# Optimization experiments

Measured on AMD Instinct MI355X. Metric: run time of the kernel, lower is better.

The kernel has to match this reference:

```python
import jax, jax.numpy as jnp
import numpy as np

PATCH = (9, 7, 5, 3)
DIM = 64
HEAD_DIM = 64
HEADS = 8
HIDDEN = 8
DEPTH = 4
SCALE = (HEAD_DIM / HEADS) ** (-0.5)  # per-head dim = 8
EPS = 1e-5


def setup_inputs() -> dict:
    key = jax.random.key(0)
    ks = jax.random.split(key, 8)
    B = 4096
    x = jax.random.normal(ks[0], (B, PATCH[0] * PATCH[0], DIM), dtype=jnp.float32)
    w_qkv = jax.random.normal(ks[1], (DEPTH, DIM, 3 * HEAD_DIM), dtype=jnp.float32) * 0.05
    b_qkv = jnp.zeros((DEPTH, 3 * HEAD_DIM), dtype=jnp.float32)
    w_o = jax.random.normal(ks[2], (DEPTH, HEAD_DIM, DIM), dtype=jnp.float32) * 0.05
    b_o = jnp.zeros((DEPTH, DIM), dtype=jnp.float32)
    ln1_g = jnp.ones((DEPTH, DIM), dtype=jnp.float32)
    ln1_b = jnp.zeros((DEPTH, DIM), dtype=jnp.float32)
    ln2_g = jnp.ones((DEPTH, DIM), dtype=jnp.float32)
    ln2_b = jnp.zeros((DEPTH, DIM), dtype=jnp.float32)
    w1 = jax.random.normal(ks[3], (DEPTH, DIM, HIDDEN), dtype=jnp.float32) * 0.05
    b1 = jnp.zeros((DEPTH, HIDDEN), dtype=jnp.float32)
    w2 = jax.random.normal(ks[4], (DEPTH, HIDDEN, DIM), dtype=jnp.float32) * 0.05
    b2 = jnp.zeros((DEPTH, DIM), dtype=jnp.float32)
    return {"x": x, "w_qkv": w_qkv, "b_qkv": b_qkv, "w_o": w_o, "b_o": b_o,
            "ln1_g": ln1_g, "ln1_b": ln1_b, "ln2_g": ln2_g, "ln2_b": ln2_b,
            "w1": w1, "b1": b1, "w2": w2, "b2": b2}


def _layernorm(x, g, b):
    m = jnp.mean(x, axis=-1, keepdims=True)
    v = jnp.mean(jnp.square(x - m), axis=-1, keepdims=True)
    return (x - m) * jax.lax.rsqrt(v + EPS) * g + b


def reference(x, w_qkv, b_qkv, w_o, b_o, ln1_g, ln1_b, ln2_g, ln2_b, w1, b1, w2, b2):
    B = x.shape[0]
    for i in range(DEPTH):
        n = x.shape[1]
        # --- attention block (Residual(Layernorm(Encoder))) ---
        y = _layernorm(x, ln1_g[i], ln1_b[i])
        qkv = y @ w_qkv[i] + b_qkv[i]                       # [B, n, 3*HEAD_DIM]
        q, k, v = jnp.split(qkv, 3, axis=-1)
        dh = HEAD_DIM // HEADS                              # 8
        q = q.reshape(B, n, HEADS, dh)
        k = k.reshape(B, n, HEADS, dh)
        v = v.reshape(B, n, HEADS, dh)
        dots = jnp.einsum('bihd,bjhd->bhij', q, k) * SCALE  # [B, H, n, n]
        attn = jax.nn.softmax(dots, axis=-1)
        out = jnp.einsum('bhij,bjhd->bihd', attn, v).reshape(B, n, HEAD_DIM)
        out = out @ w_o[i] + b_o[i]
        x = x + out                                         # dropout = identity (eval)
        # --- feedforward block ---
        y = _layernorm(x, ln2_g[i], ln2_b[i])
        h = jax.nn.gelu(y @ w1[i] + b1[i], approximate=False)
        x = x + h @ w2[i] + b2[i]
        # --- spatial pooling / rearrange ---
        p = PATCH[i]
        xg = x.reshape(B, p, p, DIM)                        # 'b (h w) d -> b h w d'
        if i != DEPTH - 1:
            xg = xg[:, 1:-1, 1:-1, :]                       # crop pool_size=1
            x = xg.reshape(B, (p - 2) * (p - 2), DIM)
        else:
            x = jnp.transpose(xg, (0, 3, 1, 2))             # 'b h w d -> b d h w'
    return x  # [B, 64, 3, 3]
```

## Files before the change

kernel.cpp:

```cpp
#include <hip/hip_runtime.h>
#include <hip/hip_bf16.h>
#include <math.h>

#define NT 512

typedef __attribute__((ext_vector_type(8))) short short8v;
typedef __attribute__((ext_vector_type(4))) short short4v;
typedef __attribute__((ext_vector_type(4))) float f32x4;
typedef __attribute__((ext_vector_type(2))) unsigned uint2v;
typedef __attribute__((ext_vector_type(4))) unsigned uint4v;

__device__ __forceinline__ unsigned short f2bf(float x) {
    unsigned u = __float_as_uint(x);
    unsigned r = ((u >> 16) & 1u) + 0x7FFFu;
    return (unsigned short)((u + r) >> 16);
}
__device__ __forceinline__ unsigned pk2(float a, float b) {
    __hip_bfloat162 h = __float22bfloat162_rn(make_float2(a, b));
    unsigned r;
    __builtin_memcpy(&r, &h, sizeof(r));
    return r;
}
__device__ __forceinline__ short bf1(float a) {
    __hip_bfloat16 h = __float2bfloat16(a);
    short r;
    __builtin_memcpy(&r, &h, sizeof(r));
    return r;
}
__device__ __forceinline__ float gelu_f(float x) {
    float x3 = x * x * x;
    float e = exp2f(-2.3022079f * x - 0.1029432f * x3);
    return x / (1.0f + e);
}
__device__ __forceinline__ f32x4 mfma32(short8v a, short8v b, f32x4 c) {
    return __builtin_amdgcn_mfma_f32_16x16x32_bf16(a, b, c, 0, 0, 0);
}

#define WS_WO 49152
#define WS_W1 65536
#define WS_W2 69632
#define WS_TOT 71680

__global__ __launch_bounds__(256) void prep_kernel(
    const float* __restrict__ w_qkv, const float* __restrict__ w_o,
    const float* __restrict__ w1, const float* __restrict__ w2,
    short* __restrict__ ws)
{
    int idx = blockIdx.x * 256 + threadIdx.x;
    if (idx < WS_WO) {
        int l = idx / 12288, r = idx % 12288, c = r >> 6, d = r & 63;
        ws[idx] = (short)f2bf(w_qkv[l * 12288 + d * 192 + c]);
    } else if (idx < WS_W1) {
        int k = idx - WS_WO; int l = k / 4096, r = k % 4096, c = r >> 6, d = r & 63;
        ws[idx] = (short)f2bf(w_o[l * 4096 + d * 64 + c]);
    } else if (idx < WS_W2) {
        int k = idx - WS_W1; int l = k / 1024, r = k % 1024, j = r >> 6, d = r & 63;
        ws[idx] = (j < 8) ? (short)f2bf(w1[l * 512 + d * 8 + j]) : (short)0;
    } else if (idx < WS_TOT) {
        int k = idx - WS_W2; int l = k / 512, r = k % 512, c = r >> 3, j = r & 7;
        ws[idx] = (short)f2bf(w2[l * 512 + j * 64 + c]);
    }
}

template<int N, int P, int L, bool LAST>
__device__ __forceinline__ void layer_fn(
    float* __restrict__ xs, short* __restrict__ ybf, short* __restrict__ qbf,
    short* __restrict__ kbf, short* __restrict__ vT,
    const short* __restrict__ ws,
    const float* __restrict__ b_qkv, const float* __restrict__ b_o,
    const float* __restrict__ ln1_g, const float* __restrict__ ln1_b,
    const float* __restrict__ ln2_g, const float* __restrict__ ln2_b,
    const float* __restrict__ b1,    const float* __restrict__ b2,
    float* __restrict__ out, int b, int t)
{
    constexpr int Mt = (N + 15) / 16;
    constexpr float SC = 0.35355339059327373f;
    const int wv = t >> 6, l = t & 63, lr = l & 15, lq = l >> 4;
    short8v zero8 = {};
    f32x4 zero4 = {0.f, 0.f, 0.f, 0.f};

    if (t < 64 * Mt) {
        const int token = t >> 2, part = t & 3, d0 = part * 16;
        short* yrow = ybf + token * 72 + d0;
        if (token < N) {
            const int row = (token / P + L) * 9 + token % P + L;
            const float* xr = xs + row * 68 + d0;
            f32x4 v[4];
            #pragma unroll
            for (int k = 0; k < 4; ++k) v[k] = *(const f32x4*)(xr + 4 * k);
            float s1 = 0.f, s2 = 0.f;
            #pragma unroll
            for (int k = 0; k < 4; ++k)
                #pragma unroll
                for (int e = 0; e < 4; ++e) { s1 += v[k][e]; s2 += v[k][e] * v[k][e]; }
            s1 += __shfl_xor(s1, 1); s2 += __shfl_xor(s2, 1);
            s1 += __shfl_xor(s1, 2); s2 += __shfl_xor(s2, 2);
            const float m = s1 * 0.015625f;
            const float r = rsqrtf(s2 * 0.015625f - m * m + 1e-5f);
            uint4v w0, w1v;
            #pragma unroll
            for (int k = 0; k < 4; ++k) {
                f32x4 g  = *(const f32x4*)&ln1_g[L * 64 + d0 + 4 * k];
                f32x4 bb = *(const f32x4*)&ln1_b[L * 64 + d0 + 4 * k];
                unsigned p0 = pk2((v[k][0]-m)*r*g[0]+bb[0], (v[k][1]-m)*r*g[1]+bb[1]);
                unsigned p1 = pk2((v[k][2]-m)*r*g[2]+bb[2], (v[k][3]-m)*r*g[3]+bb[3]);
                if (k == 0) { w0.x = p0; w0.y = p1; }
                else if (k == 1) { w0.z = p0; w0.w = p1; }
                else if (k == 2) { w1v.x = p0; w1v.y = p1; }
                else { w1v.z = p0; w1v.w = p1; }
            }
            *(uint4v*)yrow = w0;
            *(uint4v*)(yrow + 8) = w1v;
        } else {
            uint4v z = {};
            *(uint4v*)yrow = z;
            *(uint4v*)(yrow + 8) = z;
        }
    }
    __syncthreads();

    {
        const short* wqL = ws + L * 12288;
        for (int u = wv; u < Mt * 12; u += 8) {
            const int mt = u / 12, ct = u - mt * 12;
            const short* yr = &ybf[(16 * mt + lr) * 72 + lq * 8];
            short8v y0 = *(const short8v*)yr, y1 = *(const short8v*)(yr + 32);
            const short* wr = &wqL[(16 * ct + lr) * 64 + lq * 8];
            short8v w0 = *(const short8v*)wr, w1 = *(const short8v*)(wr + 32);
            if (ct < 8) {
                f32x4 acc = mfma32(w0, y0, zero4);
                acc = mfma32(w1, y1, acc);
                f32x4 bq = *(const f32x4*)&b_qkv[L * 192 + 16 * ct + lq * 4];
                const int i = 16 * mt + lr;
                if (ct < 4) {
                    unsigned p0 = pk2((acc[0]+bq[0])*SC, (acc[1]+bq[1])*SC);
                    unsigned p1 = pk2((acc[2]+bq[2])*SC, (acc[3]+bq[3])*SC);
                    unsigned* dst = (unsigned*)&qbf[i * 72 + 16 * ct + lq * 4];
                    dst[0] = p0; dst[1] = p1;
                } else {
                    unsigned p0 = pk2(acc[0]+bq[0], acc[1]+bq[1]);
                    unsigned p1 = pk2(acc[2]+bq[2], acc[3]+bq[3]);
                    unsigned* dst = (unsigned*)&kbf[i * 72 + 16 * (ct - 4) + lq * 4];
                    dst[0] = p0; dst[1] = p1;
                }
            } else {
                f32x4 acc = mfma32(y0, w0, zero4);
                acc = mfma32(y1, w1, acc);
                const int cv = 16 * (ct - 8) + lr;
                const float bias = b_qkv[L * 192 + 128 + cv];
                unsigned p0 = pk2(acc[0]+bias, acc[1]+bias);
                unsigned p1 = pk2(acc[2]+bias, acc[3]+bias);
                unsigned* dst = (unsigned*)&vT[cv * 104 + 16 * mt + lq * 4];
                dst[0] = p0; dst[1] = p1;
            }
        }
    }
    __syncthreads();

    {
        const int h = wv, hh = wv >> 1;
        short8v kf[Mt];
        #pragma unroll
        for (int jt = 0; jt < Mt; ++jt)
            kf[jt] = (l < 16) ? *(const short8v*)&kbf[(16 * jt + lr) * 72 + h * 8] : zero8;
#if __has_builtin(__builtin_amdgcn_mfma_f32_16x16x16bf16_1k)
        short4v vf[Mt];
        #pragma unroll
        for (int jt = 0; jt < Mt; ++jt)
            vf[jt] = *(const short4v*)&vT[(16 * hh + lr) * 104 + 16 * jt + lq * 4];
#else
        constexpr int KS2 = (Mt + 1) / 2;
        short8v vf8[KS2];
        #pragma unroll
        for (int ks = 0; ks < KS2; ++ks)
            vf8[ks] = *(const short8v*)&vT[(16 * hh + lr) * 104 + 32 * ks + lq * 8];
#endif
        for (int mt = 0; mt < Mt; ++mt) {
            short8v bq = (l < 16) ? *(const short8v*)&qbf[(16 * mt + lr) * 72 + h * 8] : zero8;
            f32x4 acc[Mt];
            #pragma unroll
            for (int jt = 0; jt < Mt; ++jt) acc[jt] = mfma32(kf[jt], bq, zero4);
            float psum = 0.f;
            #pragma unroll
            for (int jt = 0; jt < Mt; ++jt) {
                #pragma unroll
                for (int rg = 0; rg < 4; ++rg) {
                    const int j = 16 * jt + lq * 4 + rg;
                    float e = __expf(acc[jt][rg]);
                    e = (j < N) ? e : 0.f;
                    acc[jt][rg] = e;
                    psum += e;
                }
            }
            float den = psum + __shfl_xor(psum, 16);
            den += __shfl_xor(den, 32);
            const float dinv = 1.0f / den;
            unsigned pkk[Mt][2];
            #pragma unroll
            for (int jt = 0; jt < Mt; ++jt) {
                pkk[jt][0] = pk2(acc[jt][0] * dinv, acc[jt][1] * dinv);
                pkk[jt][1] = pk2(acc[jt][2] * dinv, acc[jt][3] * dinv);
            }
            f32x4 po = zero4;
#if __has_builtin(__builtin_amdgcn_mfma_f32_16x16x16bf16_1k)
            #pragma unroll
            for (int jt = 0; jt < Mt; ++jt) {
                uint2v pw; pw.x = pkk[jt][0]; pw.y = pkk[jt][1];
                short4v bv = __builtin_bit_cast(short4v, pw);
                po = __builtin_amdgcn_mfma_f32_16x16x16bf16_1k(vf[jt], bv, po, 0, 0, 0);
            }
#else
            #pragma unroll
            for (int ks = 0; ks < KS2; ++ks) {
                const int t1ok = (2 * ks + 1) < Mt;
                unsigned pA0 = pkk[2 * ks][0], pA1 = pkk[2 * ks][1];
                unsigned pB0 = t1ok ? pkk[2 * ks + 1][0] : 0u;
                unsigned pB1 = t1ok ? pkk[2 * ks + 1][1] : 0u;
                int i01 = ((((lq & 1) * 2) * 16) + lr) * 4;
                int i23 = ((((lq & 1) * 2 + 1) * 16) + lr) * 4;
                unsigned w0a = (unsigned)__builtin_amdgcn_ds_bpermute(i01, (int)pA0);
                unsigned w0b = (unsigned)__builtin_amdgcn_ds_bpermute(i01, (int)pB0);
                unsigned w1a = (unsigned)__builtin_amdgcn_ds_bpermute(i01, (int)pA1);
                unsigned w1b = (unsigned)__builtin_amdgcn_ds_bpermute(i01, (int)pB1);
                unsigned w2a = (unsigned)__builtin_amdgcn_ds_bpermute(i23, (int)pA0);
                unsigned w2b = (unsigned)__builtin_amdgcn_ds_bpermute(i23, (int)pB0);
                unsigned w3a = (unsigned)__builtin_amdgcn_ds_bpermute(i23, (int)pA1);
                unsigned w3b = (unsigned)__builtin_amdgcn_ds_bpermute(i23, (int)pB1);
                uint4v wv4;
                wv4.x = (lq >> 1) ? w0b : w0a;
                wv4.y = (lq >> 1) ? w1b : w1a;
                wv4.z = (lq >> 1) ? w2b : w2a;
                wv4.w = (lq >> 1) ? w3b : w3a;
                short8v bv = __builtin_bit_cast(short8v, wv4);
                po = mfma32(vf8[ks], bv, po);
            }
#endif
            if ((lq >> 1) == (h & 1)) {
                const int i = 16 * mt + lr;
                if (i < N) {
                    unsigned q0 = pk2(po[0], po[1]);
                    unsigned q1 = pk2(po[2], po[3]);
                    unsigned* dst = (unsigned*)&ybf[i * 72 + h * 8 + (lq & 1) * 4];
                    dst[0] = q0; dst[1] = q1;
                }
            }
        }
    }
    __syncthreads();

    {
        const short* woL = ws + WS_WO + L * 4096;
        for (int u = wv; u < Mt * 4; u += 8) {
            int mt = u >> 2, ct = u & 3;
            const short* ar = &ybf[(16 * mt + lr) * 72 + lq * 8];
            short8v a0 = *(const short8v*)ar;
            short8v a1 = *(const short8v*)(ar + 32);
            const short* br = &woL[(16 * ct + lr) * 64 + lq * 8];
            short8v b0 = *(const short8v*)br;
            short8v b1v = *(const short8v*)(br + 32);
            f32x4 acc = mfma32(a0, b0, zero4);
            acc = mfma32(a1, b1v, acc);
            int c = 16 * ct + lr;
            float bias = b_o[L * 64 + c];
            #pragma unroll
            for (int rg = 0; rg < 4; ++rg) {
                int i = 16 * mt + lq * 4 + rg;
                if (i < N) {
                    const int row = (i / P + L) * 9 + i % P + L;
                    xs[row * 68 + c] += acc[rg] + bias;
                }
            }
        }
    }
    __syncthreads();

    if (t < 64 * Mt) {
        const int token = t >> 2, part = t & 3, d0 = part * 16;
        short* yrow = ybf + token * 72 + d0;
        if (token < N) {
            const int row = (token / P + L) * 9 + token % P + L;
            const float* xr = xs + row * 68 + d0;
            f32x4 v[4];
            #pragma unroll
            for (int k = 0; k < 4; ++k) v[k] = *(const f32x4*)(xr + 4 * k);
            float s1 = 0.f, s2 = 0.f;
            #pragma unroll
            for (int k = 0; k < 4; ++k)
                #pragma unroll
                for (int e = 0; e < 4; ++e) { s1 += v[k][e]; s2 += v[k][e] * v[k][e]; }
            s1 += __shfl_xor(s1, 1); s2 += __shfl_xor(s2, 1);
            s1 += __shfl_xor(s1, 2); s2 += __shfl_xor(s2, 2);
            const float m = s1 * 0.015625f;
            const float r = rsqrtf(s2 * 0.015625f - m * m + 1e-5f);
            uint4v w0, w1v;
            #pragma unroll
            for (int k = 0; k < 4; ++k) {
                f32x4 g  = *(const f32x4*)&ln2_g[L * 64 + d0 + 4 * k];
                f32x4 bb = *(const f32x4*)&ln2_b[L * 64 + d0 + 4 * k];
                unsigned p0 = pk2((v[k][0]-m)*r*g[0]+bb[0], (v[k][1]-m)*r*g[1]+bb[1]);
                unsigned p1 = pk2((v[k][2]-m)*r*g[2]+bb[2], (v[k][3]-m)*r*g[3]+bb[3]);
                if (k == 0) { w0.x = p0; w0.y = p1; }
                else if (k == 1) { w0.z = p0; w0.w = p1; }
                else if (k == 2) { w1v.x = p0; w1v.y = p1; }
                else { w1v.z = p0; w1v.w = p1; }
            }
            *(uint4v*)yrow = w0;
            *(uint4v*)(yrow + 8) = w1v;
        } else {
            uint4v z = {};
            *(uint4v*)yrow = z;
            *(uint4v*)(yrow + 8) = z;
        }
    }
    __syncthreads();

    short* hb = qbf;
    {
        const short* w1L = ws + WS_W1 + L * 1024;
        for (int u = wv; u < Mt; u += 8) {
            const short* ar = &ybf[(16 * u + lr) * 72 + lq * 8];
            short8v a0 = *(const short8v*)ar;
            short8v a1 = *(const short8v*)(ar + 32);
            const short* br = &w1L[lr * 64 + lq * 8];
            short8v b0 = *(const short8v*)br;
            short8v b1v = *(const short8v*)(br + 32);
            f32x4 acc = mfma32(a0, b0, zero4);
            acc = mfma32(a1, b1v, acc);
            if (lr < 8) {
                float bg = b1[L * 8 + lr];
                #pragma unroll
                for (int rg = 0; rg < 4; ++rg)
                    hb[(16 * u + lq * 4 + rg) * 8 + lr] = bf1(gelu_f(acc[rg] + bg));
            }
        }
    }
    __syncthreads();

    {
        const short* w2L = ws + WS_W2 + L * 512;
        for (int u = wv; u < Mt * 4; u += 8) {
            int mt = u >> 2, ct = u & 3;
            short8v a = zero8, bb = zero8;
            if (l < 16) {
                a  = *(const short8v*)&hb[(16 * mt + lr) * 8];
                bb = *(const short8v*)&w2L[(16 * ct + lr) * 8];
            }
            f32x4 acc = mfma32(a, bb, zero4);
            int c = 16 * ct + lr;
            float bias = b2[L * 64 + c];
            #pragma unroll
            for (int rg = 0; rg < 4; ++rg) {
                int i = 16 * mt + lq * 4 + rg;
                if (i < N) {
                    const int row = (i / P + L) * 9 + i % P + L;
                    xs[row * 68 + c] += acc[rg] + bias;
                }
            }
        }
    }
    __syncthreads();

    if (LAST) {
        for (int idx = t; idx < 576; idx += NT) {
            const int d = idx / 9, rc = idx % 9;
            const int row = (rc / 3 + 3) * 9 + rc % 3 + 3;
            out[(size_t)b * 576 + idx] = xs[row * 68 + d];
        }
    }
}

__global__ __launch_bounds__(NT, 4) void vit_kernel(
    const float* __restrict__ x_in, const short* __restrict__ ws,
    const float* __restrict__ b_qkv, const float* __restrict__ b_o,
    const float* __restrict__ ln1_g, const float* __restrict__ ln1_b,
    const float* __restrict__ ln2_g, const float* __restrict__ ln2_b,
    const float* __restrict__ b1,    const float* __restrict__ b2,
    float* __restrict__ out)
{
    __shared__ __align__(16) float xs[81 * 68];
    __shared__ __align__(16) short ybf[96 * 72];
    __shared__ __align__(16) short qbf[96 * 72];
    __shared__ __align__(16) short kbf[96 * 72];
    __shared__ __align__(16) short vT[64 * 104];

    const int b = blockIdx.x;
    const int t = threadIdx.x;

    for (int idx = t; idx < 64 * 104; idx += NT) vT[idx] = 0;

    const float* xin = x_in + (size_t)b * 5184;
    for (int q4 = t; q4 < 1296; q4 += NT) {
        const int i = q4 >> 4, dq = q4 & 15;
        *(f32x4*)&xs[i * 68 + dq * 4] = *(const f32x4*)&xin[i * 64 + dq * 4];
    }
    __syncthreads();

    layer_fn<81, 9, 0, false>(xs, ybf, qbf, kbf, vT, ws, b_qkv, b_o,
                              ln1_g, ln1_b, ln2_g, ln2_b, b1, b2, out, b, t);
    layer_fn<49, 7, 1, false>(xs, ybf, qbf, kbf, vT, ws, b_qkv, b_o,
                              ln1_g, ln1_b, ln2_g, ln2_b, b1, b2, out, b, t);
    layer_fn<25, 5, 2, false>(xs, ybf, qbf, kbf, vT, ws, b_qkv, b_o,
                              ln1_g, ln1_b, ln2_g, ln2_b, b1, b2, out, b, t);
    layer_fn<9, 3, 3, true>(xs, ybf, qbf, kbf, vT, ws, b_qkv, b_o,
                            ln1_g, ln1_b, ln2_g, ln2_b, b1, b2, out, b, t);
}

extern "C" void kernel_launch(void* const* d_in, const int* in_sizes, int n_in,
                              void* d_out, int out_size, void* d_ws, size_t ws_size,
                              hipStream_t stream) {
    (void)n_in; (void)out_size; (void)ws_size;
    const float* x     = (const float*)d_in[0];
    const float* w_qkv = (const float*)d_in[1];
    const float* b_qkv = (const float*)d_in[2];
    const float* w_o   = (const float*)d_in[3];
    const float* b_o   = (const float*)d_in[4];
    const float* ln1_g = (const float*)d_in[5];
    const float* ln1_b = (const float*)d_in[6];
    const float* ln2_g = (const float*)d_in[7];
    const float* ln2_b = (const float*)d_in[8];
    const float* w1    = (const float*)d_in[9];
    const float* b1    = (const float*)d_in[10];
    const float* w2    = (const float*)d_in[11];
    const float* b2    = (const float*)d_in[12];
    short* ws = (short*)d_ws;

    prep_kernel<<<dim3((WS_TOT + 255) / 256), dim3(256), 0, stream>>>(w_qkv, w_o, w1, w2, ws);

    int B = in_sizes[0] / (81 * 64);
    vit_kernel<<<dim3(B), dim3(NT), 0, stream>>>(
        x, ws, b_qkv, b_o, ln1_g, ln1_b, ln2_g, ln2_b, b1, b2, (float*)d_out);
}
```

Measured before the change: 398.0 us.

## Fuse out-proj, LN2 and MLP per wave; use native exp2 for softmax and GELU

```diff
diff --git a/kernel.cpp b/kernel.cpp
--- a/kernel.cpp
+++ b/kernel.cpp
@@ -27,9 +27,16 @@
     __builtin_memcpy(&r, &h, sizeof(r));
     return r;
 }
+__device__ __forceinline__ float exp2fast(float x) {
+#if __has_builtin(__builtin_amdgcn_exp2f)
+    return __builtin_amdgcn_exp2f(x);
+#else
+    return exp2f(x);
+#endif
+}
 __device__ __forceinline__ float gelu_f(float x) {
     float x3 = x * x * x;
-    float e = exp2f(-2.3022079f * x - 0.1029432f * x3);
+    float e = exp2fast(-2.3022079f * x - 0.1029432f * x3);
     return x / (1.0f + e);
 }
 __device__ __forceinline__ f32x4 mfma32(short8v a, short8v b, f32x4 c) {
@@ -74,7 +81,7 @@
     float* __restrict__ out, int b, int t)
 {
     constexpr int Mt = (N + 15) / 16;
-    constexpr float SC = 0.35355339059327373f;
+    constexpr float SCL2E = 0.51010905835f;
     const int wv = t >> 6, l = t & 63, lr = l & 15, lq = l >> 4;
     short8v zero8 = {};
     f32x4 zero4 = {0.f, 0.f, 0.f, 0.f};
@@ -133,8 +140,8 @@
                 f32x4 bq = *(const f32x4*)&b_qkv[L * 192 + 16 * ct + lq * 4];
                 const int i = 16 * mt + lr;
                 if (ct < 4) {
-                    unsigned p0 = pk2((acc[0]+bq[0])*SC, (acc[1]+bq[1])*SC);
-                    unsigned p1 = pk2((acc[2]+bq[2])*SC, (acc[3]+bq[3])*SC);
+                    unsigned p0 = pk2((acc[0]+bq[0])*SCL2E, (acc[1]+bq[1])*SCL2E);
+                    unsigned p1 = pk2((acc[2]+bq[2])*SCL2E, (acc[3]+bq[3])*SCL2E);
                     unsigned* dst = (unsigned*)&qbf[i * 72 + 16 * ct + lq * 4];
                     dst[0] = p0; dst[1] = p1;
                 } else {
@@ -186,7 +193,7 @@
                 #pragma unroll
                 for (int rg = 0; rg < 4; ++rg) {
                     const int j = 16 * jt + lq * 4 + rg;
-                    float e = __expf(acc[jt][rg]);
+                    float e = exp2fast(acc[jt][rg]);
                     e = (j < N) ? e : 0.f;
                     acc[jt][rg] = e;
                     psum += e;
@@ -249,112 +256,83 @@
     __syncthreads();
 
     {
-        const short* woL = ws + WS_WO + L * 4096;
-        for (int u = wv; u < Mt * 4; u += 8) {
-            int mt = u >> 2, ct = u & 3;
-            const short* ar = &ybf[(16 * mt + lr) * 72 + lq * 8];
-            short8v a0 = *(const short8v*)ar;
-            short8v a1 = *(const short8v*)(ar + 32);
-            const short* br = &woL[(16 * ct + lr) * 64 + lq * 8];
-            short8v b0 = *(const short8v*)br;
-            short8v b1v = *(const short8v*)(br + 32);
-            f32x4 acc = mfma32(a0, b0, zero4);
-            acc = mfma32(a1, b1v, acc);
-            int c = 16 * ct + lr;
-            float bias = b_o[L * 64 + c];
-            #pragma unroll
-            for (int rg = 0; rg < 4; ++rg) {
-                int i = 16 * mt + lq * 4 + rg;
-                if (i < N) {
-                    const int row = (i / P + L) * 9 + i % P + L;
-                    xs[row * 68 + c] += acc[rg] + bias;
+        short* hb = qbf;
+        if (wv < Mt) {
+            const int mt = wv;
+            const int i = 16 * mt + lr;
+            const bool iok = (i < N);
+            const int xrow = iok ? (i / P + L) * 9 + (i % P) + L : 0;
+            float* xp = xs + xrow * 68;
+            const short* yr = &ybf[i * 72 + lq * 8];
+            short8v y0 = *(const short8v*)yr;
+            short8v y1 = *(const short8v*)(yr + 32);
+            const short* woL = ws + WS_WO + L * 4096;
+            f32x4 xv[4];
+            float s1 = 0.f, s2 = 0.f;
+            #pragma unroll
+            for (int ct = 0; ct < 4; ++ct) {
+                const short* wr = &woL[(16 * ct + lr) * 64 + lq * 8];
+                short8v w0 = *(const short8v*)wr, w1 = *(const short8v*)(wr + 32);
+                f32x4 acc = mfma32(w0, y0, zero4);
+                acc = mfma32(w1, y1, acc);
+                f32x4 bo = *(const f32x4*)&b_o[L * 64 + 16 * ct + 4 * lq];
+                f32x4 xc = zero4;
+                if (iok) xc = *(const f32x4*)(xp + 16 * ct + 4 * lq);
+                #pragma unroll
+                for (int rg = 0; rg < 4; ++rg) {
+                    xc[rg] += acc[rg] + bo[rg];
+                    s1 += xc[rg]; s2 += xc[rg] * xc[rg];
                 }
-            }
-        }
-    }
-    __syncthreads();
-
-    if (t < 64 * Mt) {
-        const int token = t >> 2, part = t & 3, d0 = part * 16;
-        short* yrow = ybf + token * 72 + d0;
-        if (token < N) {
-            const int row = (token / P + L) * 9 + token % P + L;
-            const float* xr = xs + row * 68 + d0;
-            f32x4 v[4];
-            #pragma unroll
-            for (int k = 0; k < 4; ++k) v[k] = *(const f32x4*)(xr + 4 * k);
-            float s1 = 0.f, s2 = 0.f;
-            #pragma unroll
-            for (int k = 0; k < 4; ++k)
-                #pragma unroll
-                for (int e = 0; e < 4; ++e) { s1 += v[k][e]; s2 += v[k][e] * v[k][e]; }
-            s1 += __shfl_xor(s1, 1); s2 += __shfl_xor(s2, 1);
-            s1 += __shfl_xor(s1, 2); s2 += __shfl_xor(s2, 2);
+                if (iok) *(f32x4*)(xp + 16 * ct + 4 * lq) = xc;
+                xv[ct] = xc;
+            }
+            s1 += __shfl_xor(s1, 16); s2 += __shfl_xor(s2, 16);
+            s1 += __shfl_xor(s1, 32); s2 += __shfl_xor(s2, 32);
             const float m = s1 * 0.015625f;
             const float r = rsqrtf(s2 * 0.015625f - m * m + 1e-5f);
-            uint4v w0, w1v;
-            #pragma unroll
-            for (int k = 0; k < 4; ++k) {
-                f32x4 g  = *(const f32x4*)&ln2_g[L * 64 + d0 + 4 * k];
-                f32x4 bb = *(const f32x4*)&ln2_b[L * 64 + d0 + 4 * k];
-                unsigned p0 = pk2((v[k][0]-m)*r*g[0]+bb[0], (v[k][1]-m)*r*g[1]+bb[1]);
-                unsigned p1 = pk2((v[k][2]-m)*r*g[2]+bb[2], (v[k][3]-m)*r*g[3]+bb[3]);
-                if (k == 0) { w0.x = p0; w0.y = p1; }
-                else if (k == 1) { w0.z = p0; w0.w = p1; }
-                else if (k == 2) { w1v.x = p0; w1v.y = p1; }
-                else { w1v.z = p0; w1v.w = p1; }
-            }
-            *(uint4v*)yrow = w0;
-            *(uint4v*)(yrow + 8) = w1v;
-        } else {
-            uint4v z = {};
-            *(uint4v*)yrow = z;
-            *(uint4v*)(yrow + 8) = z;
-        }
-    }
-    __syncthreads();
-
-    short* hb = qbf;
-    {
-        const short* w1L = ws + WS_W1 + L * 1024;
-        for (int u = wv; u < Mt; u += 8) {
-            const short* ar = &ybf[(16 * u + lr) * 72 + lq * 8];
-            short8v a0 = *(const short8v*)ar;
-            short8v a1 = *(const short8v*)(ar + 32);
-            const short* br = &w1L[lr * 64 + lq * 8];
-            short8v b0 = *(const short8v*)br;
-            short8v b1v = *(const short8v*)(br + 32);
-            f32x4 acc = mfma32(a0, b0, zero4);
-            acc = mfma32(a1, b1v, acc);
+            unsigned* ybw = (unsigned*)&ybf[i * 72];
+            #pragma unroll
+            for (int ct = 0; ct < 4; ++ct) {
+                f32x4 g  = *(const f32x4*)&ln2_g[L * 64 + 16 * ct + 4 * lq];
+                f32x4 bb = *(const f32x4*)&ln2_b[L * 64 + 16 * ct + 4 * lq];
+                ybw[8 * ct + 2 * lq]     = pk2((xv[ct][0]-m)*r*g[0]+bb[0],
+                                               (xv[ct][1]-m)*r*g[1]+bb[1]);
+                ybw[8 * ct + 2 * lq + 1] = pk2((xv[ct][2]-m)*r*g[2]+bb[2],
+                                               (xv[ct][3]-m)*r*g[3]+bb[3]);
+            }
+            uint4v ua0 = *(const uint4v*)(ybw + 4 * lq);
+            uint4v ua1 = *(const uint4v*)(ybw + 16 + 4 * lq);
+            const short* w1L = ws + WS_W1 + L * 1024;
+            short8v a10 = __builtin_bit_cast(short8v, ua0);
+            short8v a11 = __builtin_bit_cast(short8v, ua1);
+            short8v b10 = *(const short8v*)&w1L[lr * 64 + lq * 8];
+            short8v b11 = *(const short8v*)&w1L[lr * 64 + lq * 8 + 32];
+            f32x4 hA = mfma32(a10, b10, zero4);
+            hA = mfma32(a11, b11, hA);
+            const float bg = (lr < 8) ? b1[L * 8 + lr] : 0.f;
             if (lr < 8) {
-                float bg = b1[L * 8 + lr];
                 #pragma unroll
                 for (int rg = 0; rg < 4; ++rg)
-                    hb[(16 * u + lq * 4 + rg) * 8 + lr] = bf1(gelu_f(acc[rg] + bg));
-            }
-        }
-    }
-    __syncthreads();
-
-    {
-        const short* w2L = ws + WS_W2 + L * 512;
-        for (int u = wv; u < Mt * 4; u += 8) {
-            int mt = u >> 2, ct = u & 3;
-            short8v a = zero8, bb = zero8;
-            if (l < 16) {
-                a  = *(const short8v*)&hb[(16 * mt + lr) * 8];
-                bb = *(const short8v*)&w2L[(16 * ct + lr) * 8];
-            }
-            f32x4 acc = mfma32(a, bb, zero4);
-            int c = 16 * ct + lr;
-            float bias = b2[L * 64 + c];
+                    hb[(16 * mt + 4 * lq + rg) * 8 + lr] = bf1(gelu_f(hA[rg] + bg));
+            }
+            short8v ah = (lq == 0) ? *(const short8v*)&hb[(16 * mt + lr) * 8] : zero8;
+            int row2[4]; bool ok2[4];
             #pragma unroll
             for (int rg = 0; rg < 4; ++rg) {
-                int i = 16 * mt + lq * 4 + rg;
-                if (i < N) {
-                    const int row = (i / P + L) * 9 + i % P + L;
-                    xs[row * 68 + c] += acc[rg] + bias;
-                }
+                const int i2 = 16 * mt + 4 * lq + rg;
+                ok2[rg] = (i2 < N);
+                row2[rg] = ok2[rg] ? (i2 / P + L) * 9 + (i2 % P) + L : 0;
+            }
+            const short* w2L = ws + WS_W2 + L * 512;
+            #pragma unroll
+            for (int ct = 0; ct < 4; ++ct) {
+                short8v bw2 = (lq == 0) ? *(const short8v*)&w2L[(16 * ct + lr) * 8] : zero8;
+                f32x4 dacc = mfma32(ah, bw2, zero4);
+                const int c2 = 16 * ct + lr;
+                const float b2v = b2[L * 64 + c2];
+                #pragma unroll
+                for (int rg = 0; rg < 4; ++rg)
+                    if (ok2[rg]) xs[row2[rg] * 68 + c2] += dacc[rg] + b2v;
             }
         }
     }
```

Result: no change. 400.2 us (+0.5%).
